# Kernel optimization log

Measured on AMD Instinct MI355X. Metric: run time of the kernel, lower is better.

Reference implementation:

```python
import jax, jax.numpy as jnp
from jax import lax
import numpy as np

B, N_PER = 4, 8192          # equal-sized point clouds
RATIO, K = 0.5, 16
C_IN, C_OUT = 64, 128
M_PER = int(N_PER * RATIO)  # FPS samples per cloud
BN_EPS = 1e-5


def setup_inputs() -> dict:
    key = jax.random.key(0)
    k1, k2, k3 = jax.random.split(key, 3)
    N = B * N_PER
    x = jax.random.normal(k1, (N, C_IN), jnp.float32)
    pos = jax.random.uniform(k2, (N, 3), jnp.float32)
    batch = jnp.repeat(jnp.arange(B, dtype=jnp.int32), N_PER)
    W = jax.random.normal(k3, (C_IN, C_OUT), jnp.float32) / np.sqrt(C_IN).astype(np.float32)
    b = jnp.zeros((C_OUT,), jnp.float32)
    gamma = jnp.ones((C_OUT,), jnp.float32)
    beta = jnp.zeros((C_OUT,), jnp.float32)
    return {"x": x, "pos": pos, "batch": batch, "W": W, "b": b, "gamma": gamma, "beta": beta}


def _fps_single(pos_b):
    # Deterministic farthest point sampling on one cloud [N_PER, 3] -> [M_PER] indices.
    n = pos_b.shape[0]
    def step(carry, _):
        dists, last = carry
        d = jnp.sum((pos_b - pos_b[last]) ** 2, axis=-1)
        dists = jnp.minimum(dists, d)
        nxt = jnp.argmax(dists).astype(jnp.int32)
        return (dists, nxt), nxt
    init = (jnp.full((n,), jnp.inf, pos_b.dtype), jnp.int32(0))
    _, idx = lax.scan(step, init, None, length=M_PER - 1)
    return jnp.concatenate([jnp.zeros((1,), jnp.int32), idx])


def reference(x, pos, batch, W, b, gamma, beta):
    # batch is assumed to be B contiguous equal segments of N_PER points.
    pos_b = pos.reshape(B, N_PER, 3)
    samp = jax.vmap(_fps_single)(pos_b)                                # [B, M_PER]
    new_pos = jnp.take_along_axis(pos_b, samp[:, :, None], axis=1)     # [B, M_PER, 3]

    # kNN of each sampled point among all points of the same cloud (squared L2).
    sq_p = jnp.sum(pos_b * pos_b, axis=-1)                              # [B, N_PER]
    sq_q = jnp.sum(new_pos * new_pos, axis=-1)                          # [B, M_PER]
    d2 = sq_q[:, :, None] + sq_p[:, None, :] - 2.0 * jnp.einsum('bmd,bnd->bmn', new_pos, pos_b)
    _, nbr = lax.top_k(-d2, K)                                          # [B, M_PER, K]

    # MLP: Linear -> BatchNorm1d (batch stats over all N points) -> exact GELU.
    h = x @ W + b                                                       # [N, C_OUT]
    mean = jnp.mean(h, axis=0)
    var = jnp.var(h, axis=0)
    h = (h - mean) / jnp.sqrt(var + BN_EPS) * gamma + beta
    h = jax.nn.gelu(h, approximate=False)

    h_b = h.reshape(B, N_PER, C_OUT)
    gathered = jax.vmap(lambda hb, nb: hb[nb])(h_b, nbr)                # [B, M_PER, K, C_OUT]
    new_x = jnp.max(gathered, axis=2)                                   # scatter-max == max over k neighbors

    new_batch = jnp.repeat(jnp.arange(B, dtype=batch.dtype), M_PER)
    return new_x.reshape(B * M_PER, C_OUT), new_pos.reshape(B * M_PER, 3), new_batch
```

## Files before the change

### kernel.cpp

```cpp
#include <hip/hip_runtime.h>
#include <math.h>

#define NB    4
#define NPER  8192
#define MPER  4096
#define NTOT  32768
#define MTOT  16384
#define COUT  128
#define NWORK 252

#define NEWPOS_OFF 2097152
#define NEWB_OFF   2146304

#define WS_H     0u
#define WS_SAMP  16908288u
#define WS_PART  16973824u
#define WS_PART2 17006592u
#define WS_STAT  17039360u

__global__ __launch_bounds__(256) void matmul_kernel(const float* __restrict__ x,
                                                     const float* __restrict__ W,
                                                     const float* __restrict__ bias,
                                                     float* __restrict__ h) {
  __shared__ float xs[16][64];
  const int tid = threadIdx.x;
  const int rowbase = blockIdx.x * 16;
  for (int i = tid; i < 16 * 64; i += 256) xs[i >> 6][i & 63] = x[rowbase * 64 + i];
  __syncthreads();
  const int col = tid & 127;
  const int rs = (tid >> 7) * 8;
  float acc[8] = {0.f, 0.f, 0.f, 0.f, 0.f, 0.f, 0.f, 0.f};
  for (int k = 0; k < 64; ++k) {
    float wv = W[k * 128 + col];
#pragma unroll
    for (int r = 0; r < 8; ++r) acc[r] = fmaf(xs[rs + r][k], wv, acc[r]);
  }
  float bb = bias[col];
#pragma unroll
  for (int r = 0; r < 8; ++r) h[(rowbase + rs + r) * 128 + col] = acc[r] + bb;
}

__global__ __launch_bounds__(256) void stats_kernel(const float* __restrict__ h,
                                                    float* __restrict__ part,
                                                    float* __restrict__ part2) {
  const int tid = threadIdx.x;
  const int col = tid & 127;
  const int half = tid >> 7;
  const int r0 = blockIdx.x * 512;
  float s = 0.f, s2 = 0.f;
  for (int r = r0 + half; r < r0 + 512; r += 2) {
    float v = h[r * 128 + col];
    s += v;
    s2 = fmaf(v, v, s2);
  }
  __shared__ float ps[2][128], ps2[2][128];
  ps[half][col] = s;
  ps2[half][col] = s2;
  __syncthreads();
  if (half == 0) {
    part[blockIdx.x * 128 + col] = ps[0][col] + ps[1][col];
    part2[blockIdx.x * 128 + col] = ps2[0][col] + ps2[1][col];
  }
}

__global__ void finalize_kernel(const float* __restrict__ part,
                                const float* __restrict__ part2,
                                float* __restrict__ stat) {
  int col = threadIdx.x;
  float s = 0.f, s2 = 0.f;
  for (int i = 0; i < 64; ++i) {
    s += part[i * 128 + col];
    s2 += part2[i * 128 + col];
  }
  float mean = s / 32768.0f;
  float var = s2 / 32768.0f - mean * mean;
  float invstd = 1.0f / sqrtf(var + 1e-5f);
  stat[col] = mean;
  stat[128 + col] = invstd;
}

#define UMAXU(a, b) (((a) > (b)) ? (a) : (b))
#define UMINU(a, b) (((a) < (b)) ? (a) : (b))
#define DPP_FMAX(m, CTRL)                                                       \
  {                                                                             \
    int t_ = __builtin_amdgcn_update_dpp(__float_as_int(m), __float_as_int(m),  \
                                         (CTRL), 0xf, 0xf, false);              \
    m = fmaxf(m, __int_as_float(t_));                                           \
  }
#define DPP_UMIN(c, CTRL)                                                       \
  {                                                                             \
    unsigned int t_ = (unsigned int)__builtin_amdgcn_update_dpp(                \
        (int)(c), (int)(c), (CTRL), 0xf, 0xf, false);                           \
    c = UMINU(c, t_);                                                           \
  }
#define DPP_KMIN64(lo, hi, CTRL)                                                \
  {                                                                             \
    unsigned int a_ = (unsigned int)__builtin_amdgcn_update_dpp(                \
        (int)(lo), (int)(lo), (CTRL), 0xf, 0xf, false);                         \
    unsigned int b_ = (unsigned int)__builtin_amdgcn_update_dpp(                \
        (int)(hi), (int)(hi), (CTRL), 0xf, 0xf, false);                         \
    unsigned long long nk_ = ((unsigned long long)b_ << 32) | a_;               \
    unsigned long long ok_ = ((unsigned long long)(hi) << 32) | (lo);           \
    bool t_ = nk_ < ok_;                                                        \
    lo = t_ ? a_ : (lo); hi = t_ ? b_ : (hi);                                   \
  }
#define FPS_DECL(i) float px##i, py##i, pz##i, dd##i;
#define FPS_LOAD(i)                     \
  {                                     \
    const int n = tid + (i) * 512;      \
    px##i = p[n * 3 + 0];               \
    py##i = p[n * 3 + 1];               \
    pz##i = p[n * 3 + 2];               \
    dd##i = INFINITY;                   \
    lpxy[n] = make_float2(px##i, py##i);\
    lpz[n] = pz##i;                     \
  }
#define FPS_PIN(i) \
  asm volatile("" : "+v"(px##i), "+v"(py##i), "+v"(pz##i));
#define FPS_DIST(i)                                                             \
  {                                                                             \
    float dx = __fsub_rn(px##i, lx), dy = __fsub_rn(py##i, ly),                 \
          dz = __fsub_rn(pz##i, lz);                                            \
    float d = fmaf(dz, dz, fmaf(dx, dx, __fmul_rn(dy, dy)));                    \
    float nd = fminf(dd##i, d);                                                 \
    dd##i = nd;                                                                 \
    m = fmaxf(m, nd);                                                           \
  }
#define FPS_MATCH(i)                                                            \
  ci = (dd##i == D) ? (unsigned int)(tid + (i) * 512) : ci;

__global__ __launch_bounds__(512)
__attribute__((amdgpu_waves_per_eu(2, 2)))
void fused_kernel(const float* __restrict__ pos, const float* __restrict__ h,
                  int* __restrict__ samp, const float* __restrict__ stat,
                  const float* __restrict__ gamma, const float* __restrict__ beta,
                  float* __restrict__ out) {
  __shared__ __align__(16) unsigned char smem[98816];
  const int tid = threadIdx.x;
  const int wv = tid >> 6;
  if (blockIdx.x < NB) {
    const int b = blockIdx.x;
    const float* p = pos + b * NPER * 3;
    float2* lpxy = (float2*)smem;
    float* lpz = (float*)(smem + 65536);
    unsigned int* slotD = (unsigned int*)(smem + 98304);
    unsigned int* slotI = (unsigned int*)(smem + 98336);
    FPS_DECL(0) FPS_DECL(1) FPS_DECL(2) FPS_DECL(3)
    FPS_DECL(4) FPS_DECL(5) FPS_DECL(6) FPS_DECL(7)
    FPS_DECL(8) FPS_DECL(9) FPS_DECL(10) FPS_DECL(11)
    FPS_DECL(12) FPS_DECL(13) FPS_DECL(14) FPS_DECL(15)
    FPS_LOAD(0) FPS_LOAD(1) FPS_LOAD(2) FPS_LOAD(3)
    FPS_LOAD(4) FPS_LOAD(5) FPS_LOAD(6) FPS_LOAD(7)
    FPS_LOAD(8) FPS_LOAD(9) FPS_LOAD(10) FPS_LOAD(11)
    FPS_LOAD(12) FPS_LOAD(13) FPS_LOAD(14) FPS_LOAD(15)
    FPS_PIN(0) FPS_PIN(1) FPS_PIN(2) FPS_PIN(3)
    FPS_PIN(4) FPS_PIN(5) FPS_PIN(6) FPS_PIN(7)
    FPS_PIN(8) FPS_PIN(9) FPS_PIN(10) FPS_PIN(11)
    FPS_PIN(12) FPS_PIN(13) FPS_PIN(14) FPS_PIN(15)
    float lx = p[0], ly = p[1], lz = p[2];
    if (tid == 0) {
      __hip_atomic_store(&samp[b * MPER], 0, __ATOMIC_RELAXED,
                         __HIP_MEMORY_SCOPE_AGENT);
      out[NEWPOS_OFF + (b * MPER) * 3 + 0] = lx;
      out[NEWPOS_OFF + (b * MPER) * 3 + 1] = ly;
      out[NEWPOS_OFF + (b * MPER) * 3 + 2] = lz;
    }
    __syncthreads();
    for (int s = 1; s < MPER; ++s) {
      float m = 0.0f;
      FPS_DIST(0) FPS_DIST(1) FPS_DIST(2) FPS_DIST(3)
      FPS_DIST(4) FPS_DIST(5) FPS_DIST(6) FPS_DIST(7)
      FPS_DIST(8) FPS_DIST(9) FPS_DIST(10) FPS_DIST(11)
      FPS_DIST(12) FPS_DIST(13) FPS_DIST(14) FPS_DIST(15)
      DPP_FMAX(m, 0x111)
      DPP_FMAX(m, 0x112)
      DPP_FMAX(m, 0x114)
      DPP_FMAX(m, 0x118)
      DPP_FMAX(m, 0x142)
      DPP_FMAX(m, 0x143)
      if ((tid & 63) == 63) slotD[wv] = __float_as_uint(m);
      __syncthreads();
      const uint4* spD = (const uint4*)slotD;
      uint4 a0 = spD[0], a1 = spD[1];
      unsigned int r0 = UMAXU(UMAXU(a0.x, a0.y), UMAXU(a0.z, a0.w));
      unsigned int r1 = UMAXU(UMAXU(a1.x, a1.y), UMAXU(a1.z, a1.w));
      const float D = __uint_as_float(UMAXU(r0, r1));
      unsigned int ci = 0xFFFFFFFFu;
      FPS_MATCH(15) FPS_MATCH(14) FPS_MATCH(13) FPS_MATCH(12)
      FPS_MATCH(11) FPS_MATCH(10) FPS_MATCH(9) FPS_MATCH(8)
      FPS_MATCH(7) FPS_MATCH(6) FPS_MATCH(5) FPS_MATCH(4)
      FPS_MATCH(3) FPS_MATCH(2) FPS_MATCH(1) FPS_MATCH(0)
      DPP_UMIN(ci, 0x111)
      DPP_UMIN(ci, 0x112)
      DPP_UMIN(ci, 0x114)
      DPP_UMIN(ci, 0x118)
      DPP_UMIN(ci, 0x142)
      DPP_UMIN(ci, 0x143)
      if ((tid & 63) == 63) slotI[wv] = ci;
      __syncthreads();
      const uint4* spI = (const uint4*)slotI;
      uint4 b0 = spI[0], b1 = spI[1];
      unsigned int i0 = UMINU(UMINU(b0.x, b0.y), UMINU(b0.z, b0.w));
      unsigned int i1 = UMINU(UMINU(b1.x, b1.y), UMINU(b1.z, b1.w));
      const int widx = (int)UMINU(i0, i1);
      float2 wxy = lpxy[widx];
      float wz = lpz[widx];
      lx = wxy.x; ly = wxy.y; lz = wz;
      if (tid == 0) {
        __hip_atomic_store(&samp[b * MPER + s], widx, __ATOMIC_RELAXED,
                           __HIP_MEMORY_SCOPE_AGENT);
        out[NEWPOS_OFF + (b * MPER + s) * 3 + 0] = lx;
        out[NEWPOS_OFF + (b * MPER + s) * 3 + 1] = ly;
        out[NEWPOS_OFF + (b * MPER + s) * 3 + 2] = lz;
      }
    }
  } else {
    float* dist = (float*)smem;
    unsigned long long* ckey = (unsigned long long*)(smem + 32768);
    int* sidx_sh = (int*)(smem + 32768 + 128);
    const int w = (int)blockIdx.x - NB;
    {
      int g = w * 512 + tid;
      if (g < MTOT) out[NEWB_OFF + g] = (float)(g >> 12);
    }
    float bn_mean = 0.f, bn_istd = 0.f, bn_g = 0.f, bn_b = 0.f;
    if (tid < COUT) {
      bn_mean = stat[tid];
      bn_istd = stat[128 + tid];
      bn_g = gamma[tid];
      bn_b = beta[tid];
    }
    for (int j = w; j < MTOT; j += NWORK) {
      const int b = j & 3;
      const int s = j >> 2;
      const int q = (b << 12) | s;
      if (tid == 0) {
        int v;
        for (;;) {
          v = __hip_atomic_load(&samp[q], __ATOMIC_RELAXED,
                                __HIP_MEMORY_SCOPE_AGENT);
          if ((unsigned int)v < (unsigned int)NPER) break;
          __builtin_amdgcn_s_sleep(64);
        }
        sidx_sh[0] = v;
      }
      __syncthreads();
      const int sidx = sidx_sh[0];
      const int gbase = b * NPER;
      const float qx = pos[(gbase + sidx) * 3 + 0];
      const float qy = pos[(gbase + sidx) * 3 + 1];
      const float qz = pos[(gbase + sidx) * 3 + 2];
      const float sqq = fmaf(qz, qz, fmaf(qx, qx, __fmul_rn(qy, qy)));
      unsigned long long lkey = ~0ull;
      for (int i = 0; i < 16; ++i) {
        int n = tid + i * 512;
        int g = gbase + n;
        float xg = pos[g * 3 + 0], yg = pos[g * 3 + 1], zg = pos[g * 3 + 2];
        float dot = fmaf(qz, zg, fmaf(qy, yg, __fmul_rn(qx, xg)));
        float sqg = fmaf(zg, zg, fmaf(xg, xg, __fmul_rn(yg, yg)));
        float d2 = __fsub_rn(__fadd_rn(sqq, sqg), __fmul_rn(2.0f, dot));
        dist[n] = d2;
        unsigned int ub = __float_as_uint(d2);
        ub = (ub & 0x80000000u) ? ~ub : (ub | 0x80000000u);
        unsigned long long key = ((unsigned long long)ub << 32) | (unsigned int)n;
        lkey = (key < lkey) ? key : lkey;
      }
      __syncthreads();
      float mx = -INFINITY;
      for (int r = 0; r < 16; ++r) {
        const int pr = r & 1;
        unsigned int klo = (unsigned int)lkey;
        unsigned int khi = (unsigned int)(lkey >> 32);
        DPP_KMIN64(klo, khi, 0x111)
        DPP_KMIN64(klo, khi, 0x112)
        DPP_KMIN64(klo, khi, 0x114)
        DPP_KMIN64(klo, khi, 0x118)
        DPP_KMIN64(klo, khi, 0x142)
        DPP_KMIN64(klo, khi, 0x143)
        if ((tid & 63) == 63)
          ckey[pr * 8 + wv] = ((unsigned long long)khi << 32) | klo;
        __syncthreads();
        const ulonglong2* cp = (const ulonglong2*)(ckey + pr * 8);
        ulonglong2 c0 = cp[0], c1 = cp[1], c2 = cp[2], c3 = cp[3];
        unsigned long long k0 = (c0.x < c0.y) ? c0.x : c0.y;
        unsigned long long k1 = (c1.x < c1.y) ? c1.x : c1.y;
        unsigned long long k2 = (c2.x < c2.y) ? c2.x : c2.y;
        unsigned long long k3 = (c3.x < c3.y) ? c3.x : c3.y;
        k0 = (k1 < k0) ? k1 : k0;
        k2 = (k3 < k2) ? k3 : k2;
        k0 = (k2 < k0) ? k2 : k0;
        const int n = (int)(unsigned int)(k0 & 0xFFFFFFFFull);
        if (tid < COUT) {
          float v = h[(gbase + n) * 128 + tid];
          float z = (v - bn_mean) * bn_istd;
          z = z * bn_g + bn_b;
          float ge = 0.5f * z * (1.0f + erff(z * 0.70710678118654752440f));
          mx = fmaxf(mx, ge);
        }
        if (tid == (n & 511)) {
          dist[n] = INFINITY;
          lkey = ~0ull;
          for (int i = 0; i < 16; ++i) {
            int nn = tid + i * 512;
            unsigned int ub = __float_as_uint(dist[nn]);
            ub = (ub & 0x80000000u) ? ~ub : (ub | 0x80000000u);
            unsigned long long kk =
                ((unsigned long long)ub << 32) | (unsigned int)nn;
            lkey = (kk < lkey) ? kk : lkey;
          }
        }
      }
      __syncthreads();
      if (tid < COUT) out[q * 128 + tid] = mx;
    }
  }
}

extern "C" void kernel_launch(void* const* d_in, const int* in_sizes, int n_in,
                              void* d_out, int out_size, void* d_ws, size_t ws_size,
                              hipStream_t stream) {
  (void)in_sizes; (void)n_in; (void)out_size; (void)ws_size;
  const float* x     = (const float*)d_in[0];
  const float* pos   = (const float*)d_in[1];
  const float* W     = (const float*)d_in[3];
  const float* bias  = (const float*)d_in[4];
  const float* gamma = (const float*)d_in[5];
  const float* beta  = (const float*)d_in[6];
  float* out = (float*)d_out;
  char* ws = (char*)d_ws;
  float* h     = (float*)(ws + WS_H);
  int*   samp  = (int*)(ws + WS_SAMP);
  float* part  = (float*)(ws + WS_PART);
  float* part2 = (float*)(ws + WS_PART2);
  float* stat  = (float*)(ws + WS_STAT);

  matmul_kernel<<<dim3(2048), dim3(256), 0, stream>>>(x, W, bias, h);
  stats_kernel<<<dim3(64), dim3(256), 0, stream>>>(h, part, part2);
  finalize_kernel<<<dim3(1), dim3(128), 0, stream>>>(part, part2, stat);
  fused_kernel<<<dim3(256), dim3(512), 0, stream>>>(pos, h, samp, stat, gamma,
                                                    beta, out);
}
```

Before: 3.334 ms.

## Fuse linear layer and BatchNorm statistics into worker blocks overlapping FPS

Drops the separate matmul, stats and finalize kernels and moves the linear layer plus partial sum and sum-of-squares into the 252 worker blocks of the fused kernel. These run concurrently with the FPS blocks, and a global atomic counter plus a flag handshake publish the final mean and inverse std. The aim is to hide the MLP and its launches behind the serial FPS critical path. The cost is a grid-wide spin barrier that assumes every block is co-resident, an extra memset launch, and a naive per-thread dot product that rereads W from global memory.

New measurement: 3.236 ms, median of 2. 2.9% less time.

```diff
diff --git a/kernel.cpp b/kernel.cpp
--- a/kernel.cpp
+++ b/kernel.cpp
@@ -13,71 +13,11 @@
 #define NEWB_OFF   2146304
 
 #define WS_H     0u
-#define WS_SAMP  16908288u
-#define WS_PART  16973824u
-#define WS_PART2 17006592u
-#define WS_STAT  17039360u
-
-__global__ __launch_bounds__(256) void matmul_kernel(const float* __restrict__ x,
-                                                     const float* __restrict__ W,
-                                                     const float* __restrict__ bias,
-                                                     float* __restrict__ h) {
-  __shared__ float xs[16][64];
-  const int tid = threadIdx.x;
-  const int rowbase = blockIdx.x * 16;
-  for (int i = tid; i < 16 * 64; i += 256) xs[i >> 6][i & 63] = x[rowbase * 64 + i];
-  __syncthreads();
-  const int col = tid & 127;
-  const int rs = (tid >> 7) * 8;
-  float acc[8] = {0.f, 0.f, 0.f, 0.f, 0.f, 0.f, 0.f, 0.f};
-  for (int k = 0; k < 64; ++k) {
-    float wv = W[k * 128 + col];
-#pragma unroll
-    for (int r = 0; r < 8; ++r) acc[r] = fmaf(xs[rs + r][k], wv, acc[r]);
-  }
-  float bb = bias[col];
-#pragma unroll
-  for (int r = 0; r < 8; ++r) h[(rowbase + rs + r) * 128 + col] = acc[r] + bb;
-}
-
-__global__ __launch_bounds__(256) void stats_kernel(const float* __restrict__ h,
-                                                    float* __restrict__ part,
-                                                    float* __restrict__ part2) {
-  const int tid = threadIdx.x;
-  const int col = tid & 127;
-  const int half = tid >> 7;
-  const int r0 = blockIdx.x * 512;
-  float s = 0.f, s2 = 0.f;
-  for (int r = r0 + half; r < r0 + 512; r += 2) {
-    float v = h[r * 128 + col];
-    s += v;
-    s2 = fmaf(v, v, s2);
-  }
-  __shared__ float ps[2][128], ps2[2][128];
-  ps[half][col] = s;
-  ps2[half][col] = s2;
-  __syncthreads();
-  if (half == 0) {
-    part[blockIdx.x * 128 + col] = ps[0][col] + ps[1][col];
-    part2[blockIdx.x * 128 + col] = ps2[0][col] + ps2[1][col];
-  }
-}
-
-__global__ void finalize_kernel(const float* __restrict__ part,
-                                const float* __restrict__ part2,
-                                float* __restrict__ stat) {
-  int col = threadIdx.x;
-  float s = 0.f, s2 = 0.f;
-  for (int i = 0; i < 64; ++i) {
-    s += part[i * 128 + col];
-    s2 += part2[i * 128 + col];
-  }
-  float mean = s / 32768.0f;
-  float var = s2 / 32768.0f - mean * mean;
-  float invstd = 1.0f / sqrtf(var + 1e-5f);
-  stat[col] = mean;
-  stat[128 + col] = invstd;
-}
+#define WS_SAMP  16777216u
+#define WS_PART  16842752u
+#define WS_PART2 16971776u
+#define WS_STAT  17100800u
+#define WS_SYNC  17101824u
 
 #define UMAXU(a, b) (((a) > (b)) ? (a) : (b))
 #define UMINU(a, b) (((a) < (b)) ? (a) : (b))
@@ -131,9 +71,12 @@
 
 __global__ __launch_bounds__(512)
 __attribute__((amdgpu_waves_per_eu(2, 2)))
-void fused_kernel(const float* __restrict__ pos, const float* __restrict__ h,
-                  int* __restrict__ samp, const float* __restrict__ stat,
+void fused_kernel(const float* __restrict__ pos, const float* __restrict__ x,
+                  const float* __restrict__ W, const float* __restrict__ bias,
                   const float* __restrict__ gamma, const float* __restrict__ beta,
+                  float* __restrict__ h, int* __restrict__ samp,
+                  float* __restrict__ part, float* __restrict__ part2,
+                  float* __restrict__ stat, unsigned int* __restrict__ sync,
                   float* __restrict__ out) {
   __shared__ __align__(16) unsigned char smem[98816];
   const int tid = threadIdx.x;
@@ -218,11 +161,77 @@
     float* dist = (float*)smem;
     unsigned long long* ckey = (unsigned long long*)(smem + 32768);
     int* sidx_sh = (int*)(smem + 32768 + 128);
+    float* ps = (float*)(smem + 40960);
+    float* ps2 = (float*)(smem + 40960 + 2048);
     const int w = (int)blockIdx.x - NB;
+    const int col = tid & 127;
+    const int rg = tid >> 7;
     {
       int g = w * 512 + tid;
       if (g < MTOT) out[NEWB_OFF + g] = (float)(g >> 12);
     }
+    {
+      const int rbeg = w * 131;
+      int rend = rbeg + 131;
+      if (rend > NTOT) rend = NTOT;
+      float s = 0.f, s2 = 0.f;
+      const float bb = bias[col];
+      for (int base = rbeg; base < rend; base += 4) {
+        const int row = base + rg;
+        if (row < rend) {
+          const float* xr = x + row * 64;
+          float acc = 0.f;
+          for (int k = 0; k < 64; ++k) acc = fmaf(xr[k], W[k * 128 + col], acc);
+          float hv = acc + bb;
+          h[row * 128 + col] = hv;
+          s += hv;
+          s2 = fmaf(hv, hv, s2);
+        }
+      }
+      ps[rg * 128 + col] = s;
+      ps2[rg * 128 + col] = s2;
+      __syncthreads();
+      if (rg == 0) {
+        part[w * 128 + col] = ((ps[col] + ps[128 + col]) +
+                               (ps[256 + col] + ps[384 + col]));
+        part2[w * 128 + col] = ((ps2[col] + ps2[128 + col]) +
+                                (ps2[256 + col] + ps2[384 + col]));
+      }
+      __syncthreads();
+      if (tid == 0)
+        __hip_atomic_fetch_add(&sync[0], 1u, __ATOMIC_RELEASE,
+                               __HIP_MEMORY_SCOPE_AGENT);
+    }
+    if (w == 0) {
+      if (tid == 0) {
+        while (__hip_atomic_load(&sync[0], __ATOMIC_ACQUIRE,
+                                 __HIP_MEMORY_SCOPE_AGENT) < (unsigned)NWORK)
+          __builtin_amdgcn_s_sleep(16);
+      }
+      __syncthreads();
+      if (tid < COUT) {
+        float ss = 0.f, ss2 = 0.f;
+        for (int v = 0; v < NWORK; ++v) {
+          ss += part[v * 128 + tid];
+          ss2 += part2[v * 128 + tid];
+        }
+        float mean = ss / 32768.0f;
+        float var = ss2 / 32768.0f - mean * mean;
+        float invstd = 1.0f / sqrtf(var + 1e-5f);
+        stat[tid] = mean;
+        stat[128 + tid] = invstd;
+      }
+      __syncthreads();
+      if (tid == 0)
+        __hip_atomic_store(&sync[1], 0x5AFEu, __ATOMIC_RELEASE,
+                           __HIP_MEMORY_SCOPE_AGENT);
+    }
+    if (tid == 0) {
+      while (__hip_atomic_load(&sync[1], __ATOMIC_ACQUIRE,
+                               __HIP_MEMORY_SCOPE_AGENT) != 0x5AFEu)
+        __builtin_amdgcn_s_sleep(16);
+    }
+    __syncthreads();
     float bn_mean = 0.f, bn_istd = 0.f, bn_g = 0.f, bn_b = 0.f;
     if (tid < COUT) {
       bn_mean = stat[tid];
@@ -333,10 +342,10 @@
   float* part  = (float*)(ws + WS_PART);
   float* part2 = (float*)(ws + WS_PART2);
   float* stat  = (float*)(ws + WS_STAT);
-
-  matmul_kernel<<<dim3(2048), dim3(256), 0, stream>>>(x, W, bias, h);
-  stats_kernel<<<dim3(64), dim3(256), 0, stream>>>(h, part, part2);
-  finalize_kernel<<<dim3(1), dim3(128), 0, stream>>>(part, part2, stat);
-  fused_kernel<<<dim3(256), dim3(512), 0, stream>>>(pos, h, samp, stat, gamma,
-                                                    beta, out);
+  unsigned int* sync = (unsigned int*)(ws + WS_SYNC);
+
+  hipMemsetAsync(ws + WS_SYNC, 0, 8, stream);
+  fused_kernel<<<dim3(256), dim3(512), 0, stream>>>(pos, x, W, bias, gamma,
+                                                    beta, h, samp, part, part2,
+                                                    stat, sync, out);
 }
```
